# Performance work log

Hardware: AMD Instinct MI355X
Metric: run time of the kernel (lower is better)

The kernel has to match this reference:

```python
import jax, jax.numpy as jnp
import numpy as np

N, E = 50000, 800000
MUL, NATTR, NEMB, HID, NPATH = 32, 8, 8, 8, 5
AVG_NEIGH = 16.0
INV3 = 1.0 / np.sqrt(3.0)  # CG norm for 1o x 1o -> 0e (dot)
INV2 = 1.0 / np.sqrt(2.0)  # CG norm for 1o x 1o -> 1o (cross)


def setup_inputs() -> dict:
    key = jax.random.key(0)
    ks = jax.random.split(key, 16)
    f = lambda k, s: jax.random.normal(k, s, jnp.float32)
    return {
        "node_s": f(ks[0], (N, MUL)),
        "node_v": f(ks[1], (N, MUL, 3)),
        "node_attrs": f(ks[2], (N, NATTR)),
        "edge_emb": f(ks[3], (E, NEMB)),
        "edge_sh0": f(ks[4], (E, 1)),
        "edge_sh1": f(ks[5], (E, 3)),
        "W1_s": f(ks[6], (MUL, MUL)),
        "W1_v": f(ks[7], (MUL, MUL)),
        "Wm1": f(ks[8], (NEMB, HID)),
        "Wm2": f(ks[9], (HID, NPATH * MUL)),
        "W2_s": f(ks[10], (2 * MUL, MUL)),
        "W2_v": f(ks[11], (3 * MUL, MUL)),
        "Wsc_s": f(ks[12], (MUL, NATTR, MUL)),
        "Wsc_v": f(ks[13], (MUL, NATTR, MUL)),
        "edge_src": jax.random.randint(ks[14], (E,), 0, N),
        "edge_dst": jax.random.randint(ks[15], (E,), 0, N),
    }


def reference(node_s, node_v, node_attrs, edge_emb, edge_sh0, edge_sh1,
              W1_s, W1_v, Wm1, Wm2, W2_s, W2_v, Wsc_s, Wsc_v,
              edge_src, edge_dst):
    # linear_1: per-l equivariant channel mixing
    x_s = node_s @ W1_s / np.sqrt(MUL)                          # [N, MUL]
    x_v = jnp.einsum('nuc,uv->nvc', node_v, W1_v) / np.sqrt(MUL)  # [N, MUL, 3]
    # gather source node features per edge
    s = x_s[edge_src]   # [E, MUL]
    v = x_v[edge_src]   # [E, MUL, 3]
    # radial MLP on edge embedding -> per-edge UVU tensor-product weights
    h = jax.nn.silu(edge_emb @ Wm1 / np.sqrt(NEMB))
    w = (h @ Wm2 / np.sqrt(HID)).reshape(E, NPATH, MUL)
    w1, w2, w3, w4, w5 = (w[:, i] for i in range(NPATH))
    # UVU Clebsch-Gordan paths (lmax = 1)
    p1 = w1 * s * edge_sh0                                              # 0e x 0e -> 0e
    p2 = w2 * jnp.einsum('euc,ec->eu', v, edge_sh1) * INV3              # 1o x 1o -> 0e
    p3 = w3[:, :, None] * s[:, :, None] * edge_sh1[:, None, :]          # 0e x 1o -> 1o
    p4 = w4[:, :, None] * v * edge_sh0[:, :, None]                      # 1o x 0e -> 1o
    p5 = w5[:, :, None] * jnp.cross(v, edge_sh1[:, None, :]) * INV2     # 1o x 1o -> 1o
    msg_s = jnp.concatenate([p1, p2], axis=1)       # [E, 2*MUL]
    msg_v = jnp.concatenate([p3, p4, p5], axis=1)   # [E, 3*MUL, 3]
    # scatter-add messages to destination nodes
    agg_s = jax.ops.segment_sum(msg_s, edge_dst, num_segments=N)
    agg_v = jax.ops.segment_sum(msg_v, edge_dst, num_segments=N)
    inv = 1.0 / np.sqrt(AVG_NEIGH)
    agg_s = agg_s * inv
    agg_v = agg_v * inv
    # linear_2
    m_s = agg_s @ W2_s / np.sqrt(2 * MUL)
    m_v = jnp.einsum('nuc,uv->nvc', agg_v, W2_v) / np.sqrt(3 * MUL)
    # self connection: fully connected TP with scalar node attrs
    nsc = 1.0 / np.sqrt(MUL * NATTR)
    sc_s = jnp.einsum('nu,na,uav->nv', node_s, node_attrs, Wsc_s) * nsc
    sc_v = jnp.einsum('nuc,na,uav->nvc', node_v, node_attrs, Wsc_v) * nsc
    out_s = m_s + sc_s                  # [N, MUL]
    out_v = m_v + sc_v                  # [N, MUL, 3]
    return jnp.concatenate([out_s, out_v.reshape(N, MUL * 3)], axis=1)  # [N, 128]
```

## Files before the change

kernel.cpp:

```cpp
#include <hip/hip_runtime.h>
#include <math.h>

#define NN 50000
#define NE 800000
#define MUL 32
#define NPB 4
#define SCANB 49

static __device__ __forceinline__ float sigmoidf_(float v) {
    return 1.0f / (1.0f + __expf(-v));
}

typedef float f32x2 __attribute__((ext_vector_type(2)));

#define INV_SQRT_MUL   0.17677669529663687f
#define INV_SQRT_NEMB  0.35355339059327373f
#define INV_SQRT_HID   0.35355339059327373f
#define INV3C          0.5773502691896258f
#define INV2C          0.7071067811865476f
#define INV_NEIGH      0.25f
#define INV_SQRT_2MUL  0.125f
#define INV_SQRT_3MUL  0.10206207261596575f
#define NSC            0.0625f

__global__ __launch_bounds__(256) void k_node(
    const float* __restrict__ node_s, const float* __restrict__ node_v,
    const float* __restrict__ attrs,
    const float* __restrict__ W1_s, const float* __restrict__ W1_v,
    const float* __restrict__ Wsc_s, const float* __restrict__ Wsc_v,
    const int* __restrict__ edge_dst, int* __restrict__ counts,
    float* __restrict__ x, float* __restrict__ out)
{
    __shared__ float nd[NPB][136];
    __shared__ float gs[NPB][1024];
    __shared__ float gv[NPB][1024];
    const int t  = threadIdx.x;
    const int nb = blockIdx.x * NPB;

    {
        int g = blockIdx.x * 256 + t;
        if (g < NE) atomicAdd(&counts[edge_dst[g]], 1);
    }

#pragma unroll
    for (int i = t; i < NPB * 128; i += 256) {
        int nn = i >> 7, j = i & 127;
        nd[nn][j] = (j < 32) ? node_s[(nb + nn) * 32 + j]
                             : node_v[(nb + nn) * 96 + (j - 32)];
    }
    if (t < NPB * 8) nd[t >> 3][128 + (t & 7)] = attrs[(nb + (t >> 3)) * 8 + (t & 7)];
    __syncthreads();

    float at[NPB][8];
#pragma unroll
    for (int nn = 0; nn < NPB; ++nn)
#pragma unroll
        for (int a = 0; a < 8; ++a) at[nn][a] = nd[nn][128 + a];

#pragma unroll
    for (int r = 0; r < 4; ++r) {
        const int idx = t + 256 * r;
        const int u = idx >> 5, vch = idx & 31;
        float as[NPB] = {0.f, 0.f, 0.f, 0.f};
        float av[NPB] = {0.f, 0.f, 0.f, 0.f};
#pragma unroll
        for (int a = 0; a < 8; ++a) {
            const float ws = Wsc_s[(u * 8 + a) * 32 + vch];
            const float wvw = Wsc_v[(u * 8 + a) * 32 + vch];
#pragma unroll
            for (int nn = 0; nn < NPB; ++nn) {
                as[nn] += at[nn][a] * ws;
                av[nn] += at[nn][a] * wvw;
            }
        }
#pragma unroll
        for (int nn = 0; nn < NPB; ++nn) {
            gs[nn][idx] = as[nn];
            gv[nn][idx] = av[nn];
        }
    }
    __syncthreads();

    const int o  = t & 127;
    const int nh = t >> 7;
    if (o < 32) {
        float ax[2] = {0.f, 0.f}, asc[2] = {0.f, 0.f};
#pragma unroll
        for (int uu = 0; uu < 32; ++uu) {
            const float w1 = W1_s[uu * 32 + o];
#pragma unroll
            for (int r2 = 0; r2 < 2; ++r2) {
                const int nn = nh + 2 * r2;
                const float s = nd[nn][uu];
                ax[r2]  += s * w1;
                asc[r2] += s * gs[nn][(uu << 5) + o];
            }
        }
#pragma unroll
        for (int r2 = 0; r2 < 2; ++r2) {
            const int nidx = nb + nh + 2 * r2;
            x[(size_t)nidx * 128 + 4 * o] = ax[r2] * INV_SQRT_MUL;
            out[(size_t)nidx * 128 + o]   = asc[r2] * NSC;
        }
    } else {
        const int q = o - 32;
        const int vch = q / 3, c = q - 3 * vch;
        float ax[2] = {0.f, 0.f}, asc[2] = {0.f, 0.f};
#pragma unroll
        for (int uu = 0; uu < 32; ++uu) {
            const float w1 = W1_v[uu * 32 + vch];
#pragma unroll
            for (int r2 = 0; r2 < 2; ++r2) {
                const int nn = nh + 2 * r2;
                const float vv = nd[nn][32 + 3 * uu + c];
                ax[r2]  += vv * w1;
                asc[r2] += vv * gv[nn][(uu << 5) + vch];
            }
        }
#pragma unroll
        for (int r2 = 0; r2 < 2; ++r2) {
            const int nidx = nb + nh + 2 * r2;
            x[(size_t)nidx * 128 + 4 * vch + 1 + c] = ax[r2] * INV_SQRT_MUL;
            out[(size_t)nidx * 128 + o]             = asc[r2] * NSC;
        }
    }
}

__global__ __launch_bounds__(1024) void k_scan_a(
    const int* __restrict__ counts, int* __restrict__ escan,
    int* __restrict__ bsum)
{
    __shared__ int sh[1024];
    const int t = threadIdx.x;
    const int i = blockIdx.x * 1024 + t;
    int v = (i < NN) ? counts[i] : 0;
    sh[t] = v;
    __syncthreads();
    for (int off = 1; off < 1024; off <<= 1) {
        int u = (t >= off) ? sh[t - off] : 0;
        __syncthreads();
        sh[t] += u;
        __syncthreads();
    }
    if (i < NN) escan[i] = sh[t] - v;
    if (t == 1023) bsum[blockIdx.x] = sh[1023];
}

__global__ __launch_bounds__(1024) void k_scan_c(
    const int* __restrict__ escan, const int* __restrict__ bsum,
    int* __restrict__ offsets, int* __restrict__ cursor)
{
    __shared__ int sbase;
    const int t = threadIdx.x;
    if (t < 64) {
        int v = (t < blockIdx.x) ? bsum[t] : 0;
        for (int off = 32; off > 0; off >>= 1) v += __shfl_xor(v, off, 64);
        if (t == 0) sbase = v;
    }
    __syncthreads();
    const int i = blockIdx.x * 1024 + t;
    if (i == 0) offsets[NN] = NE;
    if (i < NN) {
        int o = sbase + escan[i];
        offsets[i] = o;
        cursor[i] = o;
    }
}

__global__ __launch_bounds__(256) void k_pack(
    const float* __restrict__ edge_emb, const float* __restrict__ edge_sh0,
    const float* __restrict__ edge_sh1,
    const int* __restrict__ edge_src, const int* __restrict__ edge_dst,
    const float* __restrict__ Wm1,
    int* __restrict__ cursor, float* __restrict__ epack)
{
    int e = blockIdx.x * 256 + threadIdx.x;
    if (e >= NE) return;
    const float4* p = (const float4*)(edge_emb + e * 8);
    float4 a = p[0], b = p[1];
    float emb[8] = {a.x, a.y, a.z, a.w, b.x, b.y, b.z, b.w};
    float h[8];
#pragma unroll
    for (int j = 0; j < 8; ++j) {
        float s = 0.f;
#pragma unroll
        for (int k = 0; k < 8; ++k) s += emb[k] * Wm1[k * 8 + j];
        s *= INV_SQRT_NEMB;
        h[j] = s * sigmoidf_(s);
    }
    float sh0 = edge_sh0[e];
    float sx = edge_sh1[3 * e], sy = edge_sh1[3 * e + 1], sz = edge_sh1[3 * e + 2];
    int src = edge_src[e];
    int pos = atomicAdd(&cursor[edge_dst[e]], 1);
    float4* op = (float4*)(epack + (size_t)pos * 16);
    op[0] = make_float4(__int_as_float(src), sh0, sx, sy);
    op[1] = make_float4(sz, h[0], h[1], h[2]);
    op[2] = make_float4(h[3], h[4], h[5], h[6]);
    op[3] = make_float4(h[7], 0.f, 0.f, 0.f);
}

__global__ __launch_bounds__(256) void k_gather(
    const float* __restrict__ x, const float* __restrict__ epack,
    const float* __restrict__ Wm2, const float* __restrict__ W2_s,
    const float* __restrict__ W2_v,
    const int* __restrict__ offsets, float* __restrict__ out)
{
    __shared__ float msg[4][360];

    const int w    = threadIdx.x >> 6;
    const int L    = threadIdx.x & 63;
    const int u    = L & 31;
    const int half = L >> 5;
    const int n    = blockIdx.x * 4 + w;

    f32x2 wc01[8], wc23[8];
    float wc4[8];
#pragma unroll
    for (int q = 0; q < 8; ++q) {
        wc01[q].x = Wm2[q * 160 +   0 + u] * INV_SQRT_HID;
        wc01[q].y = Wm2[q * 160 +  32 + u] * INV_SQRT_HID;
        wc23[q].x = Wm2[q * 160 +  64 + u] * INV_SQRT_HID;
        wc23[q].y = Wm2[q * 160 +  96 + u] * INV_SQRT_HID;
        wc4[q]    = Wm2[q * 160 + 128 + u] * INV_SQRT_HID;
    }

    float pa = 0.f, pb = 0.f;
    float p30 = 0.f, p31 = 0.f, p32 = 0.f;
    float p40 = 0.f, p41 = 0.f, p42 = 0.f;
    float p50 = 0.f, p51 = 0.f, p52 = 0.f;

    const int beg = offsets[n];
    const int end = offsets[n + 1];
    const int cnt = end - beg;

#define EDGE_BODY() do { \
        const float sh0 = r0.y, sx = r0.z, sy = r0.w, sz = r1.x; \
        const float hq0 = r1.y, hq1 = r1.z, hq2 = r1.w, hq3 = r2.x; \
        const float hq4 = r2.y, hq5 = r2.z, hq6 = r2.w, hq7 = h7; \
        f32x2 w01 = {0.f, 0.f}, w23 = {0.f, 0.f}; \
        w01 = __builtin_elementwise_fma((f32x2){hq0, hq0}, wc01[0], w01); \
        w23 = __builtin_elementwise_fma((f32x2){hq0, hq0}, wc23[0], w23); \
        w01 = __builtin_elementwise_fma((f32x2){hq1, hq1}, wc01[1], w01); \
        w23 = __builtin_elementwise_fma((f32x2){hq1, hq1}, wc23[1], w23); \
        w01 = __builtin_elementwise_fma((f32x2){hq2, hq2}, wc01[2], w01); \
        w23 = __builtin_elementwise_fma((f32x2){hq2, hq2}, wc23[2], w23); \
        w01 = __builtin_elementwise_fma((f32x2){hq3, hq3}, wc01[3], w01); \
        w23 = __builtin_elementwise_fma((f32x2){hq3, hq3}, wc23[3], w23); \
        w01 = __builtin_elementwise_fma((f32x2){hq4, hq4}, wc01[4], w01); \
        w23 = __builtin_elementwise_fma((f32x2){hq4, hq4}, wc23[4], w23); \
        w01 = __builtin_elementwise_fma((f32x2){hq5, hq5}, wc01[5], w01); \
        w23 = __builtin_elementwise_fma((f32x2){hq5, hq5}, wc23[5], w23); \
        w01 = __builtin_elementwise_fma((f32x2){hq6, hq6}, wc01[6], w01); \
        w23 = __builtin_elementwise_fma((f32x2){hq6, hq6}, wc23[6], w23); \
        w01 = __builtin_elementwise_fma((f32x2){hq7, hq7}, wc01[7], w01); \
        w23 = __builtin_elementwise_fma((f32x2){hq7, hq7}, wc23[7], w23); \
        const float w4 = hq0*wc4[0] + hq1*wc4[1] + hq2*wc4[2] + hq3*wc4[3] \
                       + hq4*wc4[4] + hq5*wc4[5] + hq6*wc4[6] + hq7*wc4[7]; \
        const float w0 = w01.x, w1 = w01.y, w2 = w23.x, w3 = w23.y; \
        const float ls = xv.x, lv0 = xv.y, lv1 = xv.z, lv2 = xv.w; \
        pa += w0 * (ls * sh0); \
        pb += w1 * (lv0 * sx + lv1 * sy + lv2 * sz); \
        const float t2 = w2 * ls; \
        p30 += t2 * sx; p31 += t2 * sy; p32 += t2 * sz; \
        const float t3 = w3 * sh0; \
        p40 += t3 * lv0; p41 += t3 * lv1; p42 += t3 * lv2; \
        p50 += w4 * (lv1 * sz - lv2 * sy); \
        p51 += w4 * (lv2 * sx - lv0 * sz); \
        p52 += w4 * (lv0 * sy - lv1 * sx); \
    } while (0)

#define PREFETCH(ptr) \
        const float4 q0 = ((const float4*)(ptr))[0]; \
        const float4 q1 = ((const float4*)(ptr))[1]; \
        const float4 q2 = ((const float4*)(ptr))[2]; \
        const float  qh7 = (ptr)[12]; \
        const float4 nxv = *(const float4*)(x + (size_t)__float_as_int(q0.x) * 128 + 4 * u)

#define ROTATE() do { r0 = q0; r1 = q1; r2 = q2; h7 = qh7; xv = nxv; } while (0)

    if (cnt > 0) {
        const int np = cnt >> 1;
        const float* rl = epack + (size_t)(end - 1) * 16;
        const float* r  = epack + ((size_t)beg + half) * 16;
        if (r > rl) r = rl;
        float4 r0 = ((const float4*)r)[0];
        float4 r1 = ((const float4*)r)[1];
        float4 r2 = ((const float4*)r)[2];
        float  h7 = r[12];
        float4 xv = *(const float4*)(x + (size_t)__float_as_int(r0.x) * 128 + 4 * u);

        for (int it = 0; it < np - 1; ++it) {
            r += 32;
            PREFETCH(r);
            EDGE_BODY();
            ROTATE();
        }

        if (np > 0) {
            if (cnt & 1) {
                {
                    PREFETCH(rl);
                    EDGE_BODY();
                    ROTATE();
                }
                const float mask = (half == 0) ? 1.f : 0.f;
                r0.y *= mask; r0.z *= mask; r0.w *= mask; r1.x *= mask;
                EDGE_BODY();
            } else {
                EDGE_BODY();
            }
        } else {
            const float mask = (half == 0) ? 1.f : 0.f;
            r0.y *= mask; r0.z *= mask; r0.w *= mask; r1.x *= mask;
            EDGE_BODY();
        }
    }
#undef EDGE_BODY
#undef PREFETCH
#undef ROTATE

    pa  += __shfl_xor(pa, 32);  pb  += __shfl_xor(pb, 32);
    p30 += __shfl_xor(p30, 32); p31 += __shfl_xor(p31, 32); p32 += __shfl_xor(p32, 32);
    p40 += __shfl_xor(p40, 32); p41 += __shfl_xor(p41, 32); p42 += __shfl_xor(p42, 32);
    p50 += __shfl_xor(p50, 32); p51 += __shfl_xor(p51, 32); p52 += __shfl_xor(p52, 32);

    {
        float* mg = msg[w];
        if (half == 0) {
            mg[u]              = pa  * INV_NEIGH;
            mg[32 + u]         = pb  * (INV3C * INV_NEIGH);
            mg[64 + u]         = p30 * INV_NEIGH;
            mg[64 + 96 + u]    = p31 * INV_NEIGH;
            mg[64 + 192 + u]   = p32 * INV_NEIGH;
        } else {
            mg[64 + 32 + u]        = p40 * INV_NEIGH;
            mg[64 + 96 + 32 + u]   = p41 * INV_NEIGH;
            mg[64 + 192 + 32 + u]  = p42 * INV_NEIGH;
            const float f = INV2C * INV_NEIGH;
            mg[64 + 64 + u]        = p50 * f;
            mg[64 + 96 + 64 + u]   = p51 * f;
            mg[64 + 192 + 64 + u]  = p52 * f;
        }
    }
    __syncthreads();

    {
        const int nb = blockIdx.x * 4;
        const int t = threadIdx.x;
        if (t < 128) {
            const int node = t >> 5, o = t & 31;
            float s = 0.f;
#pragma unroll
            for (int uu = 0; uu < 64; ++uu) s += msg[node][uu] * W2_s[uu * 32 + o];
            out[(size_t)(nb + node) * 128 + o] += s * INV_SQRT_2MUL;
        } else {
            const int node = (t - 128) >> 5, vch = t & 31;
            float s0 = 0.f, s1 = 0.f, s2 = 0.f;
#pragma unroll
            for (int uu = 0; uu < 96; ++uu) {
                const float wgt = W2_v[uu * 32 + vch];
                s0 += msg[node][64 + uu]       * wgt;
                s1 += msg[node][64 + 96 + uu]  * wgt;
                s2 += msg[node][64 + 192 + uu] * wgt;
            }
            float* po = out + (size_t)(nb + node) * 128 + 32 + vch * 3;
            po[0] += s0 * INV_SQRT_3MUL;
            po[1] += s1 * INV_SQRT_3MUL;
            po[2] += s2 * INV_SQRT_3MUL;
        }
    }
}

extern "C" void kernel_launch(void* const* d_in, const int* in_sizes, int n_in,
                              void* d_out, int out_size, void* d_ws, size_t ws_size,
                              hipStream_t stream) {
    const float* node_s   = (const float*)d_in[0];
    const float* node_v   = (const float*)d_in[1];
    const float* attrs    = (const float*)d_in[2];
    const float* edge_emb = (const float*)d_in[3];
    const float* edge_sh0 = (const float*)d_in[4];
    const float* edge_sh1 = (const float*)d_in[5];
    const float* W1_s     = (const float*)d_in[6];
    const float* W1_v     = (const float*)d_in[7];
    const float* Wm1      = (const float*)d_in[8];
    const float* Wm2      = (const float*)d_in[9];
    const float* W2_s     = (const float*)d_in[10];
    const float* W2_v     = (const float*)d_in[11];
    const float* Wsc_s    = (const float*)d_in[12];
    const float* Wsc_v    = (const float*)d_in[13];
    const int*   edge_src = (const int*)d_in[14];
    const int*   edge_dst = (const int*)d_in[15];
    float* out = (float*)d_out;

    float* x     = (float*)d_ws;
    float* epack = x + (size_t)NN * 128;
    int*   counts  = (int*)(epack + (size_t)NE * 16);
    int*   offsets = counts + NN;
    int*   cursor  = offsets + NN + 1;
    int*   escan   = cursor + NN;
    int*   bsum    = escan + NN;

    hipMemsetAsync(counts, 0, NN * sizeof(int), stream);

    k_node<<<NN / NPB, 256, 0, stream>>>(node_s, node_v, attrs,
                                         W1_s, W1_v, Wsc_s, Wsc_v,
                                         edge_dst, counts, x, out);
    k_scan_a<<<SCANB, 1024, 0, stream>>>(counts, escan, bsum);
    k_scan_c<<<SCANB, 1024, 0, stream>>>(escan, bsum, offsets, cursor);
    k_pack<<<(NE + 255) / 256, 256, 0, stream>>>(edge_emb, edge_sh0, edge_sh1,
                                                 edge_src, edge_dst, Wm1,
                                                 cursor, epack);
    k_gather<<<NN / 4, 256, 0, stream>>>(x, epack, Wm2, W2_s, W2_v,
                                         offsets, out);
}
```

Baseline: 401.5 us.

## Split each node's edge list across two waves in gather kernel

Each destination node's incoming edges are now split between two wavefronts, so the gather block grows to 512 threads covering the same 4 nodes. The two partial message accumulators are summed in shared memory before the linear_2 projection. This doubles the parallelism per node to hide memory latency on the edge gather. In exchange it adds an extra reduction pass and a sync, leaves half the threads idle during the projection, and may lower occupancy because of the larger blocks and doubled shared memory.

```diff
diff --git a/kernel.cpp b/kernel.cpp
--- a/kernel.cpp
+++ b/kernel.cpp
@@ -199,19 +199,21 @@
     op[3] = make_float4(h[7], 0.f, 0.f, 0.f);
 }
 
-__global__ __launch_bounds__(256) void k_gather(
+__global__ __launch_bounds__(512) void k_gather(
     const float* __restrict__ x, const float* __restrict__ epack,
     const float* __restrict__ Wm2, const float* __restrict__ W2_s,
     const float* __restrict__ W2_v,
     const int* __restrict__ offsets, float* __restrict__ out)
 {
-    __shared__ float msg[4][360];
+    __shared__ float msg[8][360];
 
     const int w    = threadIdx.x >> 6;
     const int L    = threadIdx.x & 63;
     const int u    = L & 31;
     const int half = L >> 5;
-    const int n    = blockIdx.x * 4 + w;
+    const int node = w >> 1;
+    const int aw   = w & 1;
+    const int n    = blockIdx.x * 4 + node;
 
     f32x2 wc01[8], wc23[8];
     float wc4[8];
@@ -229,9 +231,13 @@
     float p40 = 0.f, p41 = 0.f, p42 = 0.f;
     float p50 = 0.f, p51 = 0.f, p52 = 0.f;
 
-    const int beg = offsets[n];
-    const int end = offsets[n + 1];
-    const int cnt = end - beg;
+    const int beg0 = offsets[n];
+    const int end0 = offsets[n + 1];
+    const int cntT = end0 - beg0;
+    const int mid  = beg0 + ((cntT + 1) >> 1);
+    const int beg  = aw ? mid  : beg0;
+    const int end  = aw ? end0 : mid;
+    const int cnt  = end - beg;
 
 #define EDGE_BODY() do { \
         const float sh0 = r0.y, sx = r0.z, sy = r0.w, sz = r1.x; \
@@ -345,25 +351,36 @@
     __syncthreads();
 
     {
+        const int t = threadIdx.x;
+        for (int i = t; i < 4 * 352; i += 512) {
+            const int nd2 = i / 352, j = i % 352;
+            msg[2 * nd2][j] += msg[2 * nd2 + 1][j];
+        }
+    }
+    __syncthreads();
+
+    {
         const int nb = blockIdx.x * 4;
         const int t = threadIdx.x;
         if (t < 128) {
-            const int node = t >> 5, o = t & 31;
+            const int nd2 = t >> 5, o = t & 31;
+            const float* mg = msg[2 * nd2];
             float s = 0.f;
 #pragma unroll
-            for (int uu = 0; uu < 64; ++uu) s += msg[node][uu] * W2_s[uu * 32 + o];
-            out[(size_t)(nb + node) * 128 + o] += s * INV_SQRT_2MUL;
-        } else {
-            const int node = (t - 128) >> 5, vch = t & 31;
+            for (int uu = 0; uu < 64; ++uu) s += mg[uu] * W2_s[uu * 32 + o];
+            out[(size_t)(nb + nd2) * 128 + o] += s * INV_SQRT_2MUL;
+        } else if (t < 256) {
+            const int nd2 = (t - 128) >> 5, vch = t & 31;
+            const float* mg = msg[2 * nd2];
             float s0 = 0.f, s1 = 0.f, s2 = 0.f;
 #pragma unroll
             for (int uu = 0; uu < 96; ++uu) {
                 const float wgt = W2_v[uu * 32 + vch];
-                s0 += msg[node][64 + uu]       * wgt;
-                s1 += msg[node][64 + 96 + uu]  * wgt;
-                s2 += msg[node][64 + 192 + uu] * wgt;
+                s0 += mg[64 + uu]       * wgt;
+                s1 += mg[64 + 96 + uu]  * wgt;
+                s2 += mg[64 + 192 + uu] * wgt;
             }
-            float* po = out + (size_t)(nb + node) * 128 + 32 + vch * 3;
+            float* po = out + (size_t)(nb + nd2) * 128 + 32 + vch * 3;
             po[0] += s0 * INV_SQRT_3MUL;
             po[1] += s1 * INV_SQRT_3MUL;
             po[2] += s2 * INV_SQRT_3MUL;
@@ -410,6 +427,6 @@
     k_pack<<<(NE + 255) / 256, 256, 0, stream>>>(edge_emb, edge_sh0, edge_sh1,
                                                  edge_src, edge_dst, Wm1,
                                                  cursor, epack);
-    k_gather<<<NN / 4, 256, 0, stream>>>(x, epack, Wm2, W2_s, W2_v,
+    k_gather<<<NN / 4, 512, 0, stream>>>(x, epack, Wm2, W2_s, W2_v,
                                          offsets, out);
 }
```

Result: slower. 448.2 us (+11.6%).

## Make gather blocks single-wave and loop over four strided nodes

Applied to the files above, without the earlier changes.

The gather kernel now runs one 64-thread wavefront per block, which processes four nodes spaced GSTRIDE apart in sequence instead of four waves each handling one node. Each wave no longer waits at a block-wide barrier for sibling waves with different degrees, and the Wm2 register setup is amortized over four nodes. The trade-off is less parallelism per block, two barriers per node iteration, and serialized latency across the four nodes within a wave.

```diff
diff --git a/kernel.cpp b/kernel.cpp
--- a/kernel.cpp
+++ b/kernel.cpp
@@ -6,6 +6,7 @@
 #define MUL 32
 #define NPB 4
 #define SCANB 49
+#define GSTRIDE 12500
 
 static __device__ __forceinline__ float sigmoidf_(float v) {
     return 1.0f / (1.0f + __expf(-v));
@@ -199,19 +200,17 @@
     op[3] = make_float4(h[7], 0.f, 0.f, 0.f);
 }
 
-__global__ __launch_bounds__(256) void k_gather(
+__global__ __launch_bounds__(64) void k_gather(
     const float* __restrict__ x, const float* __restrict__ epack,
     const float* __restrict__ Wm2, const float* __restrict__ W2_s,
     const float* __restrict__ W2_v,
     const int* __restrict__ offsets, float* __restrict__ out)
 {
-    __shared__ float msg[4][360];
-
-    const int w    = threadIdx.x >> 6;
-    const int L    = threadIdx.x & 63;
+    __shared__ float msg[360];
+
+    const int L    = threadIdx.x;
     const int u    = L & 31;
     const int half = L >> 5;
-    const int n    = blockIdx.x * 4 + w;
 
     f32x2 wc01[8], wc23[8];
     float wc4[8];
@@ -223,15 +222,6 @@
         wc23[q].y = Wm2[q * 160 +  96 + u] * INV_SQRT_HID;
         wc4[q]    = Wm2[q * 160 + 128 + u] * INV_SQRT_HID;
     }
-
-    float pa = 0.f, pb = 0.f;
-    float p30 = 0.f, p31 = 0.f, p32 = 0.f;
-    float p40 = 0.f, p41 = 0.f, p42 = 0.f;
-    float p50 = 0.f, p51 = 0.f, p52 = 0.f;
-
-    const int beg = offsets[n];
-    const int end = offsets[n + 1];
-    const int cnt = end - beg;
 
 #define EDGE_BODY() do { \
         const float sh0 = r0.y, sx = r0.z, sy = r0.w, sz = r1.x; \
@@ -278,97 +268,103 @@
 
 #define ROTATE() do { r0 = q0; r1 = q1; r2 = q2; h7 = qh7; xv = nxv; } while (0)
 
-    if (cnt > 0) {
-        const int np = cnt >> 1;
-        const float* rl = epack + (size_t)(end - 1) * 16;
-        const float* r  = epack + ((size_t)beg + half) * 16;
-        if (r > rl) r = rl;
-        float4 r0 = ((const float4*)r)[0];
-        float4 r1 = ((const float4*)r)[1];
-        float4 r2 = ((const float4*)r)[2];
-        float  h7 = r[12];
-        float4 xv = *(const float4*)(x + (size_t)__float_as_int(r0.x) * 128 + 4 * u);
-
-        for (int it = 0; it < np - 1; ++it) {
-            r += 32;
-            PREFETCH(r);
-            EDGE_BODY();
-            ROTATE();
-        }
-
-        if (np > 0) {
-            if (cnt & 1) {
-                {
-                    PREFETCH(rl);
+    for (int k = 0; k < 4; ++k) {
+        const int n = blockIdx.x + k * GSTRIDE;
+
+        float pa = 0.f, pb = 0.f;
+        float p30 = 0.f, p31 = 0.f, p32 = 0.f;
+        float p40 = 0.f, p41 = 0.f, p42 = 0.f;
+        float p50 = 0.f, p51 = 0.f, p52 = 0.f;
+
+        const int beg = offsets[n];
+        const int end = offsets[n + 1];
+        const int cnt = end - beg;
+
+        if (cnt > 0) {
+            const int np = cnt >> 1;
+            const float* rl = epack + (size_t)(end - 1) * 16;
+            const float* r  = epack + ((size_t)beg + half) * 16;
+            if (r > rl) r = rl;
+            float4 r0 = ((const float4*)r)[0];
+            float4 r1 = ((const float4*)r)[1];
+            float4 r2 = ((const float4*)r)[2];
+            float  h7 = r[12];
+            float4 xv = *(const float4*)(x + (size_t)__float_as_int(r0.x) * 128 + 4 * u);
+
+            for (int it = 0; it < np - 1; ++it) {
+                r += 32;
+                PREFETCH(r);
+                EDGE_BODY();
+                ROTATE();
+            }
+
+            if (np > 0) {
+                if (cnt & 1) {
+                    {
+                        PREFETCH(rl);
+                        EDGE_BODY();
+                        ROTATE();
+                    }
+                    const float mask = (half == 0) ? 1.f : 0.f;
+                    r0.y *= mask; r0.z *= mask; r0.w *= mask; r1.x *= mask;
                     EDGE_BODY();
-                    ROTATE();
+                } else {
+                    EDGE_BODY();
                 }
+            } else {
                 const float mask = (half == 0) ? 1.f : 0.f;
                 r0.y *= mask; r0.z *= mask; r0.w *= mask; r1.x *= mask;
                 EDGE_BODY();
-            } else {
-                EDGE_BODY();
-            }
+            }
+        }
+
+        pa  += __shfl_xor(pa, 32);  pb  += __shfl_xor(pb, 32);
+        p30 += __shfl_xor(p30, 32); p31 += __shfl_xor(p31, 32); p32 += __shfl_xor(p32, 32);
+        p40 += __shfl_xor(p40, 32); p41 += __shfl_xor(p41, 32); p42 += __shfl_xor(p42, 32);
+        p50 += __shfl_xor(p50, 32); p51 += __shfl_xor(p51, 32); p52 += __shfl_xor(p52, 32);
+
+        if (half == 0) {
+            msg[u]              = pa  * INV_NEIGH;
+            msg[32 + u]         = pb  * (INV3C * INV_NEIGH);
+            msg[64 + u]         = p30 * INV_NEIGH;
+            msg[64 + 96 + u]    = p31 * INV_NEIGH;
+            msg[64 + 192 + u]   = p32 * INV_NEIGH;
         } else {
-            const float mask = (half == 0) ? 1.f : 0.f;
-            r0.y *= mask; r0.z *= mask; r0.w *= mask; r1.x *= mask;
-            EDGE_BODY();
-        }
+            msg[64 + 32 + u]        = p40 * INV_NEIGH;
+            msg[64 + 96 + 32 + u]   = p41 * INV_NEIGH;
+            msg[64 + 192 + 32 + u]  = p42 * INV_NEIGH;
+            const float f = INV2C * INV_NEIGH;
+            msg[64 + 64 + u]        = p50 * f;
+            msg[64 + 96 + 64 + u]   = p51 * f;
+            msg[64 + 192 + 64 + u]  = p52 * f;
+        }
+        __syncthreads();
+
+        if (L < 32) {
+            float s = 0.f;
+#pragma unroll
+            for (int uu = 0; uu < 64; ++uu) s += msg[uu] * W2_s[uu * 32 + L];
+            out[(size_t)n * 128 + L] += s * INV_SQRT_2MUL;
+        } else {
+            const int vch = L - 32;
+            float s0 = 0.f, s1 = 0.f, s2 = 0.f;
+#pragma unroll
+            for (int uu = 0; uu < 96; ++uu) {
+                const float wgt = W2_v[uu * 32 + vch];
+                s0 += msg[64 + uu]       * wgt;
+                s1 += msg[64 + 96 + uu]  * wgt;
+                s2 += msg[64 + 192 + uu] * wgt;
+            }
+            float* po = out + (size_t)n * 128 + 32 + vch * 3;
+            po[0] += s0 * INV_SQRT_3MUL;
+            po[1] += s1 * INV_SQRT_3MUL;
+            po[2] += s2 * INV_SQRT_3MUL;
+        }
+        __syncthreads();
     }
 #undef EDGE_BODY
 #undef PREFETCH
 #undef ROTATE
-
-    pa  += __shfl_xor(pa, 32);  pb  += __shfl_xor(pb, 32);
-    p30 += __shfl_xor(p30, 32); p31 += __shfl_xor(p31, 32); p32 += __shfl_xor(p32, 32);
-    p40 += __shfl_xor(p40, 32); p41 += __shfl_xor(p41, 32); p42 += __shfl_xor(p42, 32);
-    p50 += __shfl_xor(p50, 32); p51 += __shfl_xor(p51, 32); p52 += __shfl_xor(p52, 32);
-
-    {
-        float* mg = msg[w];
-        if (half == 0) {
-            mg[u]              = pa  * INV_NEIGH;
-            mg[32 + u]         = pb  * (INV3C * INV_NEIGH);
-            mg[64 + u]         = p30 * INV_NEIGH;
-            mg[64 + 96 + u]    = p31 * INV_NEIGH;
-            mg[64 + 192 + u]   = p32 * INV_NEIGH;
-        } else {
-            mg[64 + 32 + u]        = p40 * INV_NEIGH;
-            mg[64 + 96 + 32 + u]   = p41 * INV_NEIGH;
-            mg[64 + 192 + 32 + u]  = p42 * INV_NEIGH;
-            const float f = INV2C * INV_NEIGH;
-            mg[64 + 64 + u]        = p50 * f;
-            mg[64 + 96 + 64 + u]   = p51 * f;
-            mg[64 + 192 + 64 + u]  = p52 * f;
-        }
-    }
-    __syncthreads();
-
-    {
-        const int nb = blockIdx.x * 4;
-        const int t = threadIdx.x;
-        if (t < 128) {
-            const int node = t >> 5, o = t & 31;
-            float s = 0.f;
-#pragma unroll
-            for (int uu = 0; uu < 64; ++uu) s += msg[node][uu] * W2_s[uu * 32 + o];
-            out[(size_t)(nb + node) * 128 + o] += s * INV_SQRT_2MUL;
-        } else {
-            const int node = (t - 128) >> 5, vch = t & 31;
-            float s0 = 0.f, s1 = 0.f, s2 = 0.f;
-#pragma unroll
-            for (int uu = 0; uu < 96; ++uu) {
-                const float wgt = W2_v[uu * 32 + vch];
-                s0 += msg[node][64 + uu]       * wgt;
-                s1 += msg[node][64 + 96 + uu]  * wgt;
-                s2 += msg[node][64 + 192 + uu] * wgt;
-            }
-            float* po = out + (size_t)(nb + node) * 128 + 32 + vch * 3;
-            po[0] += s0 * INV_SQRT_3MUL;
-            po[1] += s1 * INV_SQRT_3MUL;
-            po[2] += s2 * INV_SQRT_3MUL;
-        }
-    }
 }
 
 extern "C" void kernel_launch(void* const* d_in, const int* in_sizes, int n_in,
@@ -410,6 +406,6 @@
     k_pack<<<(NE + 255) / 256, 256, 0, stream>>>(edge_emb, edge_sh0, edge_sh1,
                                                  edge_src, edge_dst, Wm1,
                                                  cursor, epack);
-    k_gather<<<NN / 4, 256, 0, stream>>>(x, epack, Wm2, W2_s, W2_v,
+    k_gather<<<GSTRIDE, 64, 0, stream>>>(x, epack, Wm2, W2_s, W2_v,
                                          offsets, out);
 }
```

New measurement: 975.4 us. 143% more time.
